# Performance work log

Measured on AMD Instinct MI355X. Metric: run time of the kernel, lower is better.

Reference implementation:

```python
import jax, jax.numpy as jnp
import numpy as np

SLOPE = 25.0  # fast_sigmoid surrogate slope
THRESH = 1.0
BETA = 0.8

@jax.custom_vjp
def spike_fn(x):
    # Heaviside forward, fast-sigmoid surrogate backward
    return (x > 0).astype(x.dtype)

def _spike_fwd(x):
    return spike_fn(x), x

def _spike_bwd(x, g):
    return (g / (SLOPE * jnp.abs(x) + 1.0) ** 2,)

spike_fn.defvjp(_spike_fwd, _spike_bwd)


def setup_inputs() -> dict:
    key = jax.random.key(0)
    k1, k2, k3 = jax.random.split(key, 3)
    T, B, IN, H, OUT = 1000, 256, 3, 512, 2
    x_seq = jax.random.normal(k1, (T, B, IN), dtype=jnp.float32)
    # Xavier uniform init like the torch module
    lim1 = float(np.sqrt(6.0 / (IN + H)))
    lim2 = float(np.sqrt(6.0 / (H + OUT)))
    W1 = jax.random.uniform(k2, (H, IN), minval=-lim1, maxval=lim1, dtype=jnp.float32)
    W2 = jax.random.uniform(k3, (OUT, H), minval=-lim2, maxval=lim2, dtype=jnp.float32)
    return {"x_seq": x_seq, "W1": W1, "W2": W2}


def _run_net(x_seq, W1, W2):
    # Batch the input projection across all timesteps: [T,B,H]
    cur_all = jnp.einsum("tbi,hi->tbh", x_seq, W1)
    B, H = x_seq.shape[1], W1.shape[0]
    mem0 = jnp.zeros((B, H), dtype=x_seq.dtype)

    def step(mem, cur):
        # snntorch Leaky, reset_mechanism='zero': reset from PREVIOUS mem (detached)
        reset = jax.lax.stop_gradient((mem > THRESH).astype(mem.dtype))
        mem_new = (BETA * mem + cur) * (1.0 - reset)
        spk = spike_fn(mem_new - THRESH)
        return mem_new, spk

    _, spk_rec = jax.lax.scan(step, mem0, cur_all)  # spk_rec: [T,B,H]
    # Readout only matters for the last 10 steps (avg_out = outs[-10:].mean(0))
    outs_tail = jax.nn.sigmoid(jnp.einsum("tbh,oh->tbo", spk_rec[-10:], W2))
    avg_out = outs_tail.mean(axis=0)  # [B, OUT]
    return spk_rec, avg_out


def reference(x_seq, W1, W2):
    return _run_net(x_seq, W1, W2)
```

## Files before the change

### kernel.cpp

```cpp
#include <hip/hip_runtime.h>
#include <math.h>

#define T_STEPS 1000
#define BATCH   256
#define IN_DIM  3
#define HID     512
#define OUT_DIM 2
#define BETA    0.8f
#define THRESH  1.0f
#define TAIL    10

typedef float f32x4 __attribute__((ext_vector_type(4)));

__global__ __launch_bounds__(64) void snn_main(const float* __restrict__ x,
                                               const float* __restrict__ W1,
                                               float* __restrict__ spk) {
    __shared__ float xs[T_STEPS * IN_DIM];
    const int b     = blockIdx.x >> 1;
    const int hbase = (blockIdx.x & 1) << 8;
    const int h0    = hbase + (int)threadIdx.x * 4;

    for (int k = threadIdx.x; k < T_STEPS * IN_DIM; k += 64) {
        int t = k / 3, i = k - 3 * t;
        xs[k] = x[t * (BATCH * IN_DIM) + b * IN_DIM + i];
    }
    float w[4][3];
    #pragma unroll
    for (int j = 0; j < 4; ++j)
        #pragma unroll
        for (int i = 0; i < 3; ++i)
            w[j][i] = W1[(h0 + j) * 3 + i];
    __syncthreads();

    float mem[4] = {0.0f, 0.0f, 0.0f, 0.0f};
    f32x4* op = (f32x4*)(spk + (size_t)b * HID + h0);
    #pragma unroll 2
    for (int t = 0; t < T_STEPS; ++t) {
        const float x0 = xs[t * 3 + 0];
        const float x1 = xs[t * 3 + 1];
        const float x2 = xs[t * 3 + 2];
        f32x4 s;
        #pragma unroll
        for (int j = 0; j < 4; ++j) {
            const float cur = fmaf(x0, w[j][0], fmaf(x1, w[j][1], x2 * w[j][2]));
            const float keep = (mem[j] > THRESH) ? 0.0f : 1.0f;
            mem[j] = fmaf(BETA, mem[j], cur) * keep;
            s[j] = (mem[j] > THRESH) ? 1.0f : 0.0f;
        }
        __builtin_nontemporal_store(s, op + (size_t)t * (BATCH * HID / 4));
    }
}

__global__ __launch_bounds__(640) void snn_tail(const float* __restrict__ spk,
                                                const float* __restrict__ W2,
                                                float* __restrict__ avg) {
    __shared__ float partial[TAIL][OUT_DIM];
    const int b    = blockIdx.x;
    const int wv   = threadIdx.x >> 6;
    const int lane = threadIdx.x & 63;
    const int t    = T_STEPS - TAIL + wv;

    const float* sp = spk + (size_t)t * (BATCH * HID) + b * HID;
    float s0 = 0.0f, s1 = 0.0f;
    #pragma unroll
    for (int j = 0; j < 8; ++j) {
        const int h = lane + j * 64;
        const float v = sp[h];
        s0 = fmaf(v, W2[h], s0);
        s1 = fmaf(v, W2[HID + h], s1);
    }
    #pragma unroll
    for (int off = 32; off > 0; off >>= 1) {
        s0 += __shfl_down(s0, off, 64);
        s1 += __shfl_down(s1, off, 64);
    }
    if (lane == 0) {
        partial[wv][0] = 1.0f / (1.0f + expf(-s0));
        partial[wv][1] = 1.0f / (1.0f + expf(-s1));
    }
    __syncthreads();
    if (threadIdx.x < OUT_DIM) {
        float a = 0.0f;
        #pragma unroll
        for (int i = 0; i < TAIL; ++i) a += partial[i][threadIdx.x];
        avg[b * OUT_DIM + threadIdx.x] = a * (1.0f / TAIL);
    }
}

extern "C" void kernel_launch(void* const* d_in, const int* in_sizes, int n_in,
                              void* d_out, int out_size, void* d_ws, size_t ws_size,
                              hipStream_t stream) {
    const float* x  = (const float*)d_in[0];
    const float* W1 = (const float*)d_in[1];
    const float* W2 = (const float*)d_in[2];
    float* out = (float*)d_out;
    float* spk = out;
    float* avg = out + (size_t)T_STEPS * BATCH * HID;

    snn_main<<<dim3(BATCH * 2), dim3(64), 0, stream>>>(x, W1, spk);
    snn_tail<<<dim3(BATCH), dim3(640), 0, stream>>>(spk, W2, avg);
}
```

Before: 510.5 us.

## Regroup main kernel into 256-thread blocks covering two batch rows with periodic barriers

The recurrence kernel now launches 128 blocks of 256 threads instead of 512 blocks of 64. Each block covers two full batch rows and stages both rows' inputs in shared memory. The time loop is unrolled by four and ends each group with a __syncthreads, which keeps the block's waves in lockstep so their streaming stores stay grouped. The aim is to improve write coalescing and locality for the large spike output, which is bandwidth-bound. The cost is fewer blocks on the device and extra barrier overhead.

Measured after the change: 504.3 us (median of 2 runs). About the same (-1.2%).

```diff
diff --git a/kernel.cpp b/kernel.cpp
--- a/kernel.cpp
+++ b/kernel.cpp
@@ -12,17 +12,20 @@
 
 typedef float f32x4 __attribute__((ext_vector_type(4)));
 
-__global__ __launch_bounds__(64) void snn_main(const float* __restrict__ x,
-                                               const float* __restrict__ W1,
-                                               float* __restrict__ spk) {
-    __shared__ float xs[T_STEPS * IN_DIM];
-    const int b     = blockIdx.x >> 1;
-    const int hbase = (blockIdx.x & 1) << 8;
-    const int h0    = hbase + (int)threadIdx.x * 4;
+__global__ __launch_bounds__(256) void snn_main(const float* __restrict__ x,
+                                                const float* __restrict__ W1,
+                                                float* __restrict__ spk) {
+    __shared__ float xs[2][T_STEPS * IN_DIM + 8];
+    const int bp   = blockIdx.x;
+    const int flat = (int)threadIdx.x * 4;
+    const int boff = flat >> 9;
+    const int h0   = flat & 511;
 
-    for (int k = threadIdx.x; k < T_STEPS * IN_DIM; k += 64) {
-        int t = k / 3, i = k - 3 * t;
-        xs[k] = x[t * (BATCH * IN_DIM) + b * IN_DIM + i];
+    for (int k = threadIdx.x; k < 2 * T_STEPS * IN_DIM; k += 256) {
+        int bb = k >= T_STEPS * IN_DIM;
+        int kk = k - bb * T_STEPS * IN_DIM;
+        int t = kk / 3, i = kk - 3 * t;
+        xs[bb][kk] = x[t * (BATCH * IN_DIM) + (2 * bp + bb) * IN_DIM + i];
     }
     float w[4][3];
     #pragma unroll
@@ -32,22 +35,28 @@
             w[j][i] = W1[(h0 + j) * 3 + i];
     __syncthreads();
 
+    const float* xrow = xs[boff];
     float mem[4] = {0.0f, 0.0f, 0.0f, 0.0f};
-    f32x4* op = (f32x4*)(spk + (size_t)b * HID + h0);
-    #pragma unroll 2
-    for (int t = 0; t < T_STEPS; ++t) {
-        const float x0 = xs[t * 3 + 0];
-        const float x1 = xs[t * 3 + 1];
-        const float x2 = xs[t * 3 + 2];
-        f32x4 s;
+    f32x4* op = (f32x4*)(spk + (size_t)(2 * bp) * HID + flat);
+
+    for (int t4 = 0; t4 < T_STEPS; t4 += 4) {
         #pragma unroll
-        for (int j = 0; j < 4; ++j) {
-            const float cur = fmaf(x0, w[j][0], fmaf(x1, w[j][1], x2 * w[j][2]));
-            const float keep = (mem[j] > THRESH) ? 0.0f : 1.0f;
-            mem[j] = fmaf(BETA, mem[j], cur) * keep;
-            s[j] = (mem[j] > THRESH) ? 1.0f : 0.0f;
+        for (int u = 0; u < 4; ++u) {
+            const int t = t4 + u;
+            const float x0 = xrow[t * 3 + 0];
+            const float x1 = xrow[t * 3 + 1];
+            const float x2 = xrow[t * 3 + 2];
+            f32x4 s;
+            #pragma unroll
+            for (int j = 0; j < 4; ++j) {
+                const float cur = fmaf(x0, w[j][0], fmaf(x1, w[j][1], x2 * w[j][2]));
+                const float keep = (mem[j] > THRESH) ? 0.0f : 1.0f;
+                mem[j] = fmaf(BETA, mem[j], cur) * keep;
+                s[j] = (mem[j] > THRESH) ? 1.0f : 0.0f;
+            }
+            __builtin_nontemporal_store(s, op + (size_t)t * (BATCH * HID / 4));
         }
-        __builtin_nontemporal_store(s, op + (size_t)t * (BATCH * HID / 4));
+        __syncthreads();
     }
 }
 
@@ -97,6 +106,6 @@
     float* spk = out;
     float* avg = out + (size_t)T_STEPS * BATCH * HID;
 
-    snn_main<<<dim3(BATCH * 2), dim3(64), 0, stream>>>(x, W1, spk);
+    snn_main<<<dim3(BATCH / 2), dim3(256), 0, stream>>>(x, W1, spk);
     snn_tail<<<dim3(BATCH), dim3(640), 0, stream>>>(spk, W2, avg);
 }
```

## Split recurrence into ballot-packed spike bits plus separate float expansion kernel

Applied to the files above, without the earlier changes.

The recurrence kernel now runs one hidden unit per thread (512 threads per batch row) and packs spikes into 64-bit ballot masks written to workspace. A new expansion kernel reads the bitmasks and writes the full float spike tensor with coalesced vector stores over a large grid. This decouples the serial time loop from the 512MB output write so the write can run at full bandwidth across all CUs. It adds an extra launch and a small workspace round trip, and drops the nontemporal store hint.

Measured after the change: 613.2 us. +20.1%, slower.

```diff
diff --git a/kernel.cpp b/kernel.cpp
--- a/kernel.cpp
+++ b/kernel.cpp
@@ -12,42 +12,57 @@
 
 typedef float f32x4 __attribute__((ext_vector_type(4)));
 
-__global__ __launch_bounds__(64) void snn_main(const float* __restrict__ x,
-                                               const float* __restrict__ W1,
-                                               float* __restrict__ spk) {
+__global__ __launch_bounds__(512) void snn_spikes(const float* __restrict__ x,
+                                                  const float* __restrict__ W1,
+                                                  unsigned long long* __restrict__ bits) {
     __shared__ float xs[T_STEPS * IN_DIM];
-    const int b     = blockIdx.x >> 1;
-    const int hbase = (blockIdx.x & 1) << 8;
-    const int h0    = hbase + (int)threadIdx.x * 4;
+    const int b  = blockIdx.x;
+    const int h  = threadIdx.x;
+    const int wv = h >> 6;
 
-    for (int k = threadIdx.x; k < T_STEPS * IN_DIM; k += 64) {
+    for (int k = threadIdx.x; k < T_STEPS * IN_DIM; k += 512) {
         int t = k / 3, i = k - 3 * t;
         xs[k] = x[t * (BATCH * IN_DIM) + b * IN_DIM + i];
     }
-    float w[4][3];
-    #pragma unroll
-    for (int j = 0; j < 4; ++j)
-        #pragma unroll
-        for (int i = 0; i < 3; ++i)
-            w[j][i] = W1[(h0 + j) * 3 + i];
+    const float w0 = W1[h * 3 + 0];
+    const float w1 = W1[h * 3 + 1];
+    const float w2 = W1[h * 3 + 2];
     __syncthreads();
 
-    float mem[4] = {0.0f, 0.0f, 0.0f, 0.0f};
-    f32x4* op = (f32x4*)(spk + (size_t)b * HID + h0);
+    float mem = 0.0f;
+    unsigned long long* wp = bits + (size_t)b * 8 + wv;
     #pragma unroll 2
     for (int t = 0; t < T_STEPS; ++t) {
-        const float x0 = xs[t * 3 + 0];
-        const float x1 = xs[t * 3 + 1];
-        const float x2 = xs[t * 3 + 2];
-        f32x4 s;
+        const float cur = fmaf(xs[3 * t + 0], w0,
+                          fmaf(xs[3 * t + 1], w1, xs[3 * t + 2] * w2));
+        const float keep = (mem > THRESH) ? 0.0f : 1.0f;
+        mem = fmaf(BETA, mem, cur) * keep;
+        const unsigned long long m = __ballot(mem > THRESH);
+        if ((h & 63) == 0) wp[(size_t)t * (BATCH * HID / 64)] = m;
+    }
+}
+
+__global__ __launch_bounds__(256) void snn_expand(const unsigned long long* __restrict__ bits,
+                                                  float* __restrict__ spk) {
+    const int NREG = T_STEPS * BATCH * HID / 4096;
+    const int T   = threadIdx.x;
+    const int sub = T & 15;
+    const int wrd = T >> 4;
+
+    for (int reg = blockIdx.x; reg < NREG; reg += gridDim.x) {
+        const unsigned long long* wb = bits + (size_t)reg * 64;
+        float* op = spk + (size_t)reg * 4096;
         #pragma unroll
-        for (int j = 0; j < 4; ++j) {
-            const float cur = fmaf(x0, w[j][0], fmaf(x1, w[j][1], x2 * w[j][2]));
-            const float keep = (mem[j] > THRESH) ? 0.0f : 1.0f;
-            mem[j] = fmaf(BETA, mem[j], cur) * keep;
-            s[j] = (mem[j] > THRESH) ? 1.0f : 0.0f;
+        for (int r = 0; r < 4; ++r) {
+            const unsigned long long m = wb[r * 16 + wrd];
+            const unsigned nib = (unsigned)(m >> (sub * 4)) & 0xFu;
+            f32x4 v;
+            v.x = (nib & 1u) ? 1.0f : 0.0f;
+            v.y = (nib & 2u) ? 1.0f : 0.0f;
+            v.z = (nib & 4u) ? 1.0f : 0.0f;
+            v.w = (nib & 8u) ? 1.0f : 0.0f;
+            *(f32x4*)(op + r * 1024 + T * 4) = v;
         }
-        __builtin_nontemporal_store(s, op + (size_t)t * (BATCH * HID / 4));
     }
 }
 
@@ -96,7 +111,9 @@
     float* out = (float*)d_out;
     float* spk = out;
     float* avg = out + (size_t)T_STEPS * BATCH * HID;
+    unsigned long long* bits = (unsigned long long*)d_ws;
 
-    snn_main<<<dim3(BATCH * 2), dim3(64), 0, stream>>>(x, W1, spk);
-    snn_tail<<<dim3(BATCH), dim3(640), 0, stream>>>(spk, W2, avg);
+    snn_spikes<<<dim3(BATCH), dim3(512), 0, stream>>>(x, W1, bits);
+    snn_expand<<<dim3(2048), dim3(256), 0, stream>>>(bits, spk);
+    snn_tail  <<<dim3(BATCH), dim3(640), 0, stream>>>(spk, W2, avg);
 }
```
